# Kernel optimization log

Measured on AMD Instinct MI355X. Metric: run time of the kernel, lower is better.

The kernel has to match this reference:

```python
import jax, jax.numpy as jnp
import numpy as np

N = 50000   # input points
M = 50000   # output points
C = 32      # in_channels
H = 128     # hidden_dim
O = 64      # out_channels
E = 1_600_000  # total neighbor pairs (avg degree 32)


def setup_inputs() -> dict:
    key = jax.random.key(0)
    ks = jax.random.split(key, 6)
    in_features = jax.random.normal(ks[0], (N, C), jnp.float32)
    out_features = jax.random.normal(ks[1], (M, C), jnp.float32)
    neighbors_index = jax.random.randint(ks[2], (E,), 0, N, dtype=jnp.int32)
    rs = jnp.sort(jax.random.randint(ks[3], (M + 1,), 0, E, dtype=jnp.int32))
    neighbors_row_splits = rs.at[0].set(0).at[-1].set(E)
    W1 = jax.random.normal(ks[4], (2 * C, H), jnp.float32) / np.float32(np.sqrt(2 * C))
    b1 = jnp.zeros((H,), jnp.float32)
    W2 = jax.random.normal(ks[5], (H, O), jnp.float32) / np.float32(np.sqrt(H))
    b2 = jnp.zeros((O,), jnp.float32)
    return dict(in_features=in_features, out_features=out_features,
                W1=W1, b1=b1, W2=W2, b2=b2,
                neighbors_index=neighbors_index,
                neighbors_row_splits=neighbors_row_splits)


def reference(in_features, out_features, W1, b1, W2, b2,
              neighbors_index, neighbors_row_splits):
    rs = neighbors_row_splits
    counts = rs[1:] - rs[:-1]                      # [M] neighbors per output point
    # segment id of each edge: largest s with rs[s] <= e (handles empty segments)
    seg_ids = jnp.searchsorted(rs, jnp.arange(E, dtype=rs.dtype), side='right') - 1
    rep = in_features[neighbors_index]             # [E, C] gathered neighbor feats
    slf = out_features[seg_ids]                    # [E, C] == repeat_interleave(out, counts)
    agg = jnp.concatenate([rep, slf], axis=1)      # [E, 2C]
    h = jax.nn.gelu(agg @ W1 + b1, approximate=False)  # torch.nn.GELU is exact erf
    y = h @ W2 + b2                                # [E, O]
    summed = jax.ops.segment_sum(y, seg_ids, num_segments=M)  # [M, O]
    denom = jnp.maximum(counts, 1).astype(summed.dtype)[:, None]
    return summed / denom                          # segment_csr 'mean' (0 for empty)
```

## Files before the change

kernel.cpp:

```cpp
#include <hip/hip_runtime.h>
#include <hip/hip_bf16.h>

typedef __bf16 bf16_t;
typedef __attribute__((ext_vector_type(8))) __bf16 bf16x8;
typedef __attribute__((ext_vector_type(4))) float f32x4;
typedef __attribute__((ext_vector_type(4))) float float4_t;

#define MFMA16(a, b, c) __builtin_amdgcn_mfma_f32_16x16x32_bf16((a), (b), (c), 0, 0, 0)

__device__ __forceinline__ float gelu_fast(float x) {
    float z = x * fmaf(x * x, -0.1029453f, -2.3022081f);
    float e = __builtin_amdgcn_exp2f(z);
    return x * __builtin_amdgcn_rcpf(1.0f + e);
}

__device__ __forceinline__ int lbound(const int* __restrict__ a, int n, int v) {
    int lo = 0, hi = n;
    while (lo < hi) { int mid = (lo + hi) >> 1; if (a[mid] < v) lo = mid + 1; else hi = mid; }
    return lo;
}

__global__ __launch_bounds__(256, 2)
void nmlp_kernel(const float* __restrict__ in_f, const float* __restrict__ out_f,
                 const float* __restrict__ W1, const float* __restrict__ b1,
                 const float* __restrict__ W2, const float* __restrict__ b2,
                 const int* __restrict__ nbr, const int* __restrict__ rsp,
                 float* __restrict__ out, int M, int E, int epw)
{
    __shared__ alignas(16) unsigned char lds[32768];
    float* wstage = (float*)lds;
    const int tid = threadIdx.x, lane = tid & 63, wslot = tid >> 6;
    const int g = lane >> 4, c = lane & 15;

    {
        const float4_t* src = (const float4_t*)W1;
        float4_t* dst = (float4_t*)wstage;
        #pragma unroll
        for (int i = 0; i < 8; ++i) dst[tid + 256 * i] = src[tid + 256 * i];
    }
    __syncthreads();
    bf16x8 w1f[8][2];
    #pragma unroll
    for (int t = 0; t < 8; ++t)
        #pragma unroll
        for (int k = 0; k < 2; ++k)
            #pragma unroll
            for (int j = 0; j < 8; ++j)
                w1f[t][k][j] = (bf16_t)wstage[(32 * k + 8 * g + j) * 128 + 16 * t + c];
    __syncthreads();
    {
        const float4_t* src = (const float4_t*)W2;
        float4_t* dst = (float4_t*)wstage;
        #pragma unroll
        for (int i = 0; i < 8; ++i) dst[tid + 256 * i] = src[tid + 256 * i];
    }
    __syncthreads();
    bf16x8 w2f[4][4];
    #pragma unroll
    for (int u = 0; u < 4; ++u)
        #pragma unroll
        for (int k = 0; k < 4; ++k)
            #pragma unroll
            for (int j = 0; j < 8; ++j)
                w2f[u][k][j] = (bf16_t)wstage[(32 * k + 8 * g + j) * 64 + 16 * u + c];
    __syncthreads();

    float b1r[8], b2r[4];
    #pragma unroll
    for (int t = 0; t < 8; ++t) b1r[t] = b1[16 * t + c];
    #pragma unroll
    for (int u = 0; u < 4; ++u) b2r[u] = b2[16 * u + c];

    const unsigned hbase = (unsigned)wslot * 4352u;
    const unsigned hwb = hbase + (unsigned)(g * 1088 + 2 * c);
    const unsigned hrb = hbase + (unsigned)(c * 272 + 16 * g);

    const int wid = blockIdx.x * 4 + wslot;
    int sA = lbound(rsp, M + 1, wid * epw);
    int sB = lbound(rsp, M + 1, wid * epw + epw);
    if (sA > M) sA = M;
    if (sB > M) sB = M;
    if (sA >= sB) return;

    int s = sA;
    int e0c = rsp[s], e1c = rsp[s + 1];
    const int eS = e0c, eE = rsp[sB];

    f32x4 colacc[4];
    #pragma unroll
    for (int u = 0; u < 4; ++u) colacc[u] = (f32x4){0.f, 0.f, 0.f, 0.f};

    if (eS < eE) {
        int er = eS + c; if (er > eE - 1) er = eE - 1;
        int nb = nbr[er];
        int sg;
        { int lo2 = s, hi2 = sB - 1;
          while (lo2 < hi2) { int mid = (lo2 + hi2 + 1) >> 1; if (rsp[mid] <= er) lo2 = mid; else hi2 = mid - 1; }
          sg = lo2; }
        float4_t f0, f1, g0, g1;
        { const float4_t* rp = (const float4_t*)(in_f + (size_t)nb * 32 + 8 * g); f0 = rp[0]; f1 = rp[1]; }
        { const float4_t* sp = (const float4_t*)(out_f + (size_t)sg * 32 + 8 * g); g0 = sp[0]; g1 = sp[1]; }

        for (int et = eS; et < eE; et += 16) {
            const bool more = (et + 16 < eE);
            int nbN = 0, sgN = 0;
            if (more) {
                int erN = et + 16 + c; if (erN > eE - 1) erN = eE - 1;
                nbN = nbr[erN];
                int lo2 = s, hi2 = sB - 1;
                while (lo2 < hi2) { int mid = (lo2 + hi2 + 1) >> 1; if (rsp[mid] <= erN) lo2 = mid; else hi2 = mid - 1; }
                sgN = lo2;
            }
            bf16x8 a0, a1;
            #pragma unroll
            for (int j = 0; j < 4; ++j) {
                a0[j] = (bf16_t)f0[j]; a0[4 + j] = (bf16_t)f1[j];
                a1[j] = (bf16_t)g0[j]; a1[4 + j] = (bf16_t)g1[j];
            }
            #pragma unroll
            for (int t = 0; t < 8; ++t) {
                f32x4 h = {b1r[t], b1r[t], b1r[t], b1r[t]};
                h = MFMA16(a0, w1f[t][0], h);
                h = MFMA16(a1, w1f[t][1], h);
                #pragma unroll
                for (int j = 0; j < 4; ++j)
                    *(bf16_t*)(lds + hwb + j * 272 + t * 32) = (bf16_t)gelu_fast(h[j]);
            }
            if (more) {
                const float4_t* rp = (const float4_t*)(in_f + (size_t)nbN * 32 + 8 * g); f0 = rp[0]; f1 = rp[1];
                const float4_t* sp = (const float4_t*)(out_f + (size_t)sgN * 32 + 8 * g); g0 = sp[0]; g1 = sp[1];
            }
            const int tend = (et + 16 < eE) ? et + 16 : eE;
            const bool pure = (e0c <= et) && (e1c >= et + 16) && (et + 16 <= eE);
            if (pure) {
                #pragma unroll
                for (int k2 = 0; k2 < 4; ++k2) {
                    bf16x8 ah = *(const bf16x8*)(lds + hrb + k2 * 64);
                    #pragma unroll
                    for (int u = 0; u < 4; ++u) colacc[u] = MFMA16(ah, w2f[u][k2], colacc[u]);
                }
                while (e1c <= tend) {
                    const int d = e1c - e0c;
                    const float inv = (d > 0) ? __builtin_amdgcn_rcpf((float)d) : 0.0f;
                    float* orow = out + (size_t)s * 64;
                    #pragma unroll
                    for (int u = 0; u < 4; ++u) {
                        float v = colacc[u][0] + colacc[u][1] + colacc[u][2] + colacc[u][3];
                        v += __shfl_xor(v, 16); v += __shfl_xor(v, 32);
                        if (g == 0) orow[u * 16 + c] = (d > 0) ? v * inv + b2r[u] : 0.0f;
                        colacc[u] = (f32x4){0.f, 0.f, 0.f, 0.f};
                    }
                    ++s; e0c = e1c;
                    if (s >= sB) break;
                    e1c = rsp[s + 1];
                }
            } else {
                f32x4 y[4];
                #pragma unroll
                for (int u = 0; u < 4; ++u) y[u] = (f32x4){0.f, 0.f, 0.f, 0.f};
                #pragma unroll
                for (int k2 = 0; k2 < 4; ++k2) {
                    bf16x8 ah = *(const bf16x8*)(lds + hrb + k2 * 64);
                    #pragma unroll
                    for (int u = 0; u < 4; ++u) y[u] = MFMA16(ah, w2f[u][k2], y[u]);
                }
                while (true) {
                    int hi_p = ((e1c < tend) ? e1c : tend) - et;
                    int lo_p = e0c - et; if (lo_p < 0) lo_p = 0;
                    float m[4];
                    #pragma unroll
                    for (int j = 0; j < 4; ++j) {
                        int r = 4 * g + j;
                        m[j] = (r >= lo_p && r < hi_p) ? 1.0f : 0.0f;
                    }
                    #pragma unroll
                    for (int u = 0; u < 4; ++u)
                        #pragma unroll
                        for (int j = 0; j < 4; ++j)
                            colacc[u][j] = fmaf(y[u][j], m[j], colacc[u][j]);
                    if (e1c <= tend) {
                        const int d = e1c - e0c;
                        const float inv = (d > 0) ? __builtin_amdgcn_rcpf((float)d) : 0.0f;
                        float* orow = out + (size_t)s * 64;
                        #pragma unroll
                        for (int u = 0; u < 4; ++u) {
                            float v = colacc[u][0] + colacc[u][1] + colacc[u][2] + colacc[u][3];
                            v += __shfl_xor(v, 16); v += __shfl_xor(v, 32);
                            if (g == 0) orow[u * 16 + c] = (d > 0) ? v * inv + b2r[u] : 0.0f;
                            colacc[u] = (f32x4){0.f, 0.f, 0.f, 0.f};
                        }
                        ++s; e0c = e1c;
                        if (s >= sB) break;
                        e1c = rsp[s + 1];
                    } else break;
                }
            }
        }
    }
    while (s < sB) {
        float* orow = out + (size_t)s * 64;
        if (g == 0) {
            #pragma unroll
            for (int u = 0; u < 4; ++u) orow[u * 16 + c] = 0.0f;
        }
        ++s;
    }
}

extern "C" void kernel_launch(void* const* d_in, const int* in_sizes, int n_in,
                              void* d_out, int out_size, void* d_ws, size_t ws_size,
                              hipStream_t stream) {
    const float* in_f  = (const float*)d_in[0];
    const float* out_f = (const float*)d_in[1];
    const float* W1    = (const float*)d_in[2];
    const float* b1    = (const float*)d_in[3];
    const float* W2    = (const float*)d_in[4];
    const float* b2    = (const float*)d_in[5];
    const int*   nbr   = (const int*)d_in[6];
    const int*   rsp   = (const int*)d_in[7];
    float* out = (float*)d_out;
    const int M = in_sizes[7] - 1;
    const int E = in_sizes[6];

    const int nblocks = 1024;
    const int nwaves  = nblocks * 4;
    const int epw = (E + nwaves - 1) / nwaves;

    nmlp_kernel<<<dim3(nblocks), dim3(256), 0, stream>>>(in_f, out_f, W1, b1, W2, b2,
                                                         nbr, rsp, out, M, E, epw);
}
```

Before: 182.4 us.

## Keep weights in LDS in MFMA layout and process two 16-edge tiles per iteration

Weights are now stored as pre-swizzled bf16 fragments in LDS rather than held in registers. The MFMA operands are transposed so the hidden activations stay in registers and feed the second matmul directly, with no LDS round-trip. Each iteration processes two 16-edge tiles, and occupancy is raised to 3 blocks/SM with 768 blocks. The aim is lower register pressure, removal of the hidden-layer LDS staging and barrier traffic, and more memory latency hiding, at the cost of extra LDS weight reads per tile and a shuffle-based reduction at segment close.

```diff
diff --git a/kernel.cpp b/kernel.cpp
--- a/kernel.cpp
+++ b/kernel.cpp
@@ -20,188 +20,162 @@
     return lo;
 }
 
-__global__ __launch_bounds__(256, 2)
+__device__ __forceinline__ int seg_of(const int* __restrict__ rsp, int lo, int hi, int er) {
+    while (lo < hi) { int mid = (lo + hi + 1) >> 1; if (rsp[mid] <= er) lo = mid; else hi = mid - 1; }
+    return lo;
+}
+
+__global__ __launch_bounds__(256, 3)
 void nmlp_kernel(const float* __restrict__ in_f, const float* __restrict__ out_f,
                  const float* __restrict__ W1, const float* __restrict__ b1,
                  const float* __restrict__ W2, const float* __restrict__ b2,
                  const int* __restrict__ nbr, const int* __restrict__ rsp,
-                 float* __restrict__ out, int M, int E, int epw)
+                 float* __restrict__ out, int M, int E, int epw, int nwaves)
 {
-    __shared__ alignas(16) unsigned char lds[32768];
-    float* wstage = (float*)lds;
+    __shared__ alignas(16) unsigned char lds[33536];
     const int tid = threadIdx.x, lane = tid & 63, wslot = tid >> 6;
     const int g = lane >> 4, c = lane & 15;
 
-    {
-        const float4_t* src = (const float4_t*)W1;
-        float4_t* dst = (float4_t*)wstage;
-        #pragma unroll
-        for (int i = 0; i < 8; ++i) dst[tid + 256 * i] = src[tid + 256 * i];
-    }
+    for (int i = 0; i < 32; ++i) {
+        int idx = i * 256 + tid;
+        int k = idx >> 7, n = idx & 127;
+        int ks = k >> 5, gg = (k >> 3) & 3, j = k & 7, t = n >> 4, cc = n & 15;
+        ((bf16_t*)lds)[(((2 * t + ks) * 4 + gg) * 16 + cc) * 8 + j] = (bf16_t)W1[idx];
+    }
+    for (int i = 0; i < 32; ++i) {
+        int idx = i * 256 + tid;
+        int l = idx >> 6, o = idx & 63;
+        int t = l >> 4, gg = (l >> 2) & 3, j = l & 3;
+        int k2 = t >> 1, j2 = (t & 1) * 4 + j, u = o >> 4, cc = o & 15;
+        ((bf16_t*)lds)[8192 + (((u * 4 + k2) * 4 + gg) * 16 + cc) * 8 + j2] = (bf16_t)W2[idx];
+    }
+    if (tid < 128) *(float*)(lds + 32768 + tid * 4) = b1[tid];
+    if (tid < 64)  *(float*)(lds + 33280 + tid * 4) = b2[tid];
     __syncthreads();
-    bf16x8 w1f[8][2];
-    #pragma unroll
-    for (int t = 0; t < 8; ++t)
-        #pragma unroll
-        for (int k = 0; k < 2; ++k)
-            #pragma unroll
-            for (int j = 0; j < 8; ++j)
-                w1f[t][k][j] = (bf16_t)wstage[(32 * k + 8 * g + j) * 128 + 16 * t + c];
-    __syncthreads();
-    {
-        const float4_t* src = (const float4_t*)W2;
-        float4_t* dst = (float4_t*)wstage;
-        #pragma unroll
-        for (int i = 0; i < 8; ++i) dst[tid + 256 * i] = src[tid + 256 * i];
-    }
-    __syncthreads();
-    bf16x8 w2f[4][4];
-    #pragma unroll
-    for (int u = 0; u < 4; ++u)
-        #pragma unroll
-        for (int k = 0; k < 4; ++k)
-            #pragma unroll
-            for (int j = 0; j < 8; ++j)
-                w2f[u][k][j] = (bf16_t)wstage[(32 * k + 8 * g + j) * 64 + 16 * u + c];
-    __syncthreads();
-
-    float b1r[8], b2r[4];
-    #pragma unroll
-    for (int t = 0; t < 8; ++t) b1r[t] = b1[16 * t + c];
-    #pragma unroll
-    for (int u = 0; u < 4; ++u) b2r[u] = b2[16 * u + c];
-
-    const unsigned hbase = (unsigned)wslot * 4352u;
-    const unsigned hwb = hbase + (unsigned)(g * 1088 + 2 * c);
-    const unsigned hrb = hbase + (unsigned)(c * 272 + 16 * g);
+
+    const unsigned wbase = (unsigned)lane * 16u;
 
     const int wid = blockIdx.x * 4 + wslot;
     int sA = lbound(rsp, M + 1, wid * epw);
     int sB = lbound(rsp, M + 1, wid * epw + epw);
     if (sA > M) sA = M;
     if (sB > M) sB = M;
+    if (wid == nwaves - 1) sB = M;
     if (sA >= sB) return;
 
-    int s = sA;
-    int e0c = rsp[s], e1c = rsp[s + 1];
+    int s = sA, e0c = rsp[s], e1c = rsp[s + 1];
     const int eS = e0c, eE = rsp[sB];
 
     f32x4 colacc[4];
     #pragma unroll
     for (int u = 0; u < 4; ++u) colacc[u] = (f32x4){0.f, 0.f, 0.f, 0.f};
 
-    if (eS < eE) {
-        int er = eS + c; if (er > eE - 1) er = eE - 1;
-        int nb = nbr[er];
-        int sg;
-        { int lo2 = s, hi2 = sB - 1;
-          while (lo2 < hi2) { int mid = (lo2 + hi2 + 1) >> 1; if (rsp[mid] <= er) lo2 = mid; else hi2 = mid - 1; }
-          sg = lo2; }
-        float4_t f0, f1, g0, g1;
-        { const float4_t* rp = (const float4_t*)(in_f + (size_t)nb * 32 + 8 * g); f0 = rp[0]; f1 = rp[1]; }
-        { const float4_t* sp = (const float4_t*)(out_f + (size_t)sg * 32 + 8 * g); g0 = sp[0]; g1 = sp[1]; }
-
-        for (int et = eS; et < eE; et += 16) {
-            const bool more = (et + 16 < eE);
-            int nbN = 0, sgN = 0;
-            if (more) {
-                int erN = et + 16 + c; if (erN > eE - 1) erN = eE - 1;
-                nbN = nbr[erN];
-                int lo2 = s, hi2 = sB - 1;
-                while (lo2 < hi2) { int mid = (lo2 + hi2 + 1) >> 1; if (rsp[mid] <= erN) lo2 = mid; else hi2 = mid - 1; }
-                sgN = lo2;
-            }
-            bf16x8 a0, a1;
-            #pragma unroll
-            for (int j = 0; j < 4; ++j) {
-                a0[j] = (bf16_t)f0[j]; a0[4 + j] = (bf16_t)f1[j];
-                a1[j] = (bf16_t)g0[j]; a1[4 + j] = (bf16_t)g1[j];
-            }
-            #pragma unroll
-            for (int t = 0; t < 8; ++t) {
-                f32x4 h = {b1r[t], b1r[t], b1r[t], b1r[t]};
-                h = MFMA16(a0, w1f[t][0], h);
-                h = MFMA16(a1, w1f[t][1], h);
+    auto accum_close = [&](int bt, const f32x4* y) {
+        const int tend = (bt + 16 < eE) ? bt + 16 : eE;
+        const int er = bt + c;
+        while (true) {
+            int hi_p = (e1c < tend) ? e1c : tend;
+            int lo_p = (e0c > bt) ? e0c : bt;
+            float m = (er >= lo_p && er < hi_p) ? 1.0f : 0.0f;
+            #pragma unroll
+            for (int u = 0; u < 4; ++u)
                 #pragma unroll
                 for (int j = 0; j < 4; ++j)
-                    *(bf16_t*)(lds + hwb + j * 272 + t * 32) = (bf16_t)gelu_fast(h[j]);
-            }
-            if (more) {
-                const float4_t* rp = (const float4_t*)(in_f + (size_t)nbN * 32 + 8 * g); f0 = rp[0]; f1 = rp[1];
-                const float4_t* sp = (const float4_t*)(out_f + (size_t)sgN * 32 + 8 * g); g0 = sp[0]; g1 = sp[1];
-            }
-            const int tend = (et + 16 < eE) ? et + 16 : eE;
-            const bool pure = (e0c <= et) && (e1c >= et + 16) && (et + 16 <= eE);
-            if (pure) {
-                #pragma unroll
-                for (int k2 = 0; k2 < 4; ++k2) {
-                    bf16x8 ah = *(const bf16x8*)(lds + hrb + k2 * 64);
-                    #pragma unroll
-                    for (int u = 0; u < 4; ++u) colacc[u] = MFMA16(ah, w2f[u][k2], colacc[u]);
-                }
-                while (e1c <= tend) {
-                    const int d = e1c - e0c;
-                    const float inv = (d > 0) ? __builtin_amdgcn_rcpf((float)d) : 0.0f;
-                    float* orow = out + (size_t)s * 64;
-                    #pragma unroll
-                    for (int u = 0; u < 4; ++u) {
-                        float v = colacc[u][0] + colacc[u][1] + colacc[u][2] + colacc[u][3];
-                        v += __shfl_xor(v, 16); v += __shfl_xor(v, 32);
-                        if (g == 0) orow[u * 16 + c] = (d > 0) ? v * inv + b2r[u] : 0.0f;
-                        colacc[u] = (f32x4){0.f, 0.f, 0.f, 0.f};
-                    }
-                    ++s; e0c = e1c;
-                    if (s >= sB) break;
-                    e1c = rsp[s + 1];
-                }
-            } else {
-                f32x4 y[4];
-                #pragma unroll
-                for (int u = 0; u < 4; ++u) y[u] = (f32x4){0.f, 0.f, 0.f, 0.f};
-                #pragma unroll
-                for (int k2 = 0; k2 < 4; ++k2) {
-                    bf16x8 ah = *(const bf16x8*)(lds + hrb + k2 * 64);
-                    #pragma unroll
-                    for (int u = 0; u < 4; ++u) y[u] = MFMA16(ah, w2f[u][k2], y[u]);
-                }
-                while (true) {
-                    int hi_p = ((e1c < tend) ? e1c : tend) - et;
-                    int lo_p = e0c - et; if (lo_p < 0) lo_p = 0;
-                    float m[4];
+                    colacc[u][j] = fmaf(y[u][j], m, colacc[u][j]);
+            if (e1c <= tend) {
+                const int d = e1c - e0c;
+                const float inv = (d > 0) ? __builtin_amdgcn_rcpf((float)d) : 0.0f;
+                float* orow = out + (size_t)s * 64;
+                #pragma unroll
+                for (int u = 0; u < 4; ++u) {
+                    const f32x4 b2v = *(const f32x4*)(lds + 33280 + u * 64 + g * 16);
                     #pragma unroll
                     for (int j = 0; j < 4; ++j) {
-                        int r = 4 * g + j;
-                        m[j] = (r >= lo_p && r < hi_p) ? 1.0f : 0.0f;
+                        float v = colacc[u][j];
+                        v += __shfl_xor(v, 1); v += __shfl_xor(v, 2);
+                        v += __shfl_xor(v, 4); v += __shfl_xor(v, 8);
+                        if (c == 0) orow[u * 16 + g * 4 + j] = (d > 0) ? fmaf(v, inv, b2v[j]) : 0.0f;
                     }
-                    #pragma unroll
-                    for (int u = 0; u < 4; ++u)
-                        #pragma unroll
-                        for (int j = 0; j < 4; ++j)
-                            colacc[u][j] = fmaf(y[u][j], m[j], colacc[u][j]);
-                    if (e1c <= tend) {
-                        const int d = e1c - e0c;
-                        const float inv = (d > 0) ? __builtin_amdgcn_rcpf((float)d) : 0.0f;
-                        float* orow = out + (size_t)s * 64;
-                        #pragma unroll
-                        for (int u = 0; u < 4; ++u) {
-                            float v = colacc[u][0] + colacc[u][1] + colacc[u][2] + colacc[u][3];
-                            v += __shfl_xor(v, 16); v += __shfl_xor(v, 32);
-                            if (g == 0) orow[u * 16 + c] = (d > 0) ? v * inv + b2r[u] : 0.0f;
-                            colacc[u] = (f32x4){0.f, 0.f, 0.f, 0.f};
-                        }
-                        ++s; e0c = e1c;
-                        if (s >= sB) break;
-                        e1c = rsp[s + 1];
-                    } else break;
+                    colacc[u] = (f32x4){0.f, 0.f, 0.f, 0.f};
                 }
-            }
+                ++s; e0c = e1c;
+                if (s >= sB) break;
+                e1c = rsp[s + 1];
+            } else break;
+        }
+    };
+
+    if (eS < eE) {
+        int erA = eS + c;      if (erA > eE - 1) erA = eE - 1;
+        int erB = eS + 16 + c; if (erB > eE - 1) erB = eE - 1;
+        int nbA = nbr[erA], nbB = nbr[erB];
+        int sgA = seg_of(rsp, s, sB - 1, erA), sgB = seg_of(rsp, s, sB - 1, erB);
+        float4_t fA0, fA1, gA0, gA1, fB0, fB1, gB0, gB1;
+        { const float4_t* p = (const float4_t*)(in_f  + (size_t)nbA * 32 + 8 * g); fA0 = p[0]; fA1 = p[1]; }
+        { const float4_t* p = (const float4_t*)(out_f + (size_t)sgA * 32 + 8 * g); gA0 = p[0]; gA1 = p[1]; }
+        { const float4_t* p = (const float4_t*)(in_f  + (size_t)nbB * 32 + 8 * g); fB0 = p[0]; fB1 = p[1]; }
+        { const float4_t* p = (const float4_t*)(out_f + (size_t)sgB * 32 + 8 * g); gB0 = p[0]; gB1 = p[1]; }
+
+        for (int et = eS; et < eE; et += 32) {
+            bf16x8 aA0, aA1, aB0, aB1;
+            #pragma unroll
+            for (int j = 0; j < 4; ++j) {
+                aA0[j] = (bf16_t)fA0[j]; aA0[4 + j] = (bf16_t)fA1[j];
+                aA1[j] = (bf16_t)gA0[j]; aA1[4 + j] = (bf16_t)gA1[j];
+                aB0[j] = (bf16_t)fB0[j]; aB0[4 + j] = (bf16_t)fB1[j];
+                aB1[j] = (bf16_t)gB0[j]; aB1[4 + j] = (bf16_t)gB1[j];
+            }
+            const bool more = (et + 32 < eE);
+            int nbA2 = 0, sgA2 = 0, nbB2 = 0, sgB2 = 0;
+            if (more) {
+                int eA2 = et + 32 + c; if (eA2 > eE - 1) eA2 = eE - 1;
+                int eB2 = et + 48 + c; if (eB2 > eE - 1) eB2 = eE - 1;
+                nbA2 = nbr[eA2]; nbB2 = nbr[eB2];
+                sgA2 = seg_of(rsp, s, sB - 1, eA2); sgB2 = seg_of(rsp, s, sB - 1, eB2);
+            }
+            bf16x8 phA[4], phB[4];
+            #pragma unroll
+            for (int t = 0; t < 8; ++t) {
+                const f32x4 b1v  = *(const f32x4*)(lds + 32768 + t * 64 + g * 16);
+                const bf16x8 w10 = *(const bf16x8*)(lds + wbase + (2 * t) * 1024);
+                const bf16x8 w11 = *(const bf16x8*)(lds + wbase + (2 * t + 1) * 1024);
+                f32x4 hA = b1v, hB = b1v;
+                hA = MFMA16(w10, aA0, hA); hA = MFMA16(w11, aA1, hA);
+                hB = MFMA16(w10, aB0, hB); hB = MFMA16(w11, aB1, hB);
+                #pragma unroll
+                for (int j = 0; j < 4; ++j) {
+                    phA[t >> 1][(t & 1) * 4 + j] = (bf16_t)gelu_fast(hA[j]);
+                    phB[t >> 1][(t & 1) * 4 + j] = (bf16_t)gelu_fast(hB[j]);
+                }
+            }
+            if (more) {
+                { const float4_t* p = (const float4_t*)(in_f  + (size_t)nbA2 * 32 + 8 * g); fA0 = p[0]; fA1 = p[1]; }
+                { const float4_t* p = (const float4_t*)(out_f + (size_t)sgA2 * 32 + 8 * g); gA0 = p[0]; gA1 = p[1]; }
+                { const float4_t* p = (const float4_t*)(in_f  + (size_t)nbB2 * 32 + 8 * g); fB0 = p[0]; fB1 = p[1]; }
+                { const float4_t* p = (const float4_t*)(out_f + (size_t)sgB2 * 32 + 8 * g); gB0 = p[0]; gB1 = p[1]; }
+            }
+            f32x4 yA[4], yB[4];
+            #pragma unroll
+            for (int u = 0; u < 4; ++u) { yA[u] = (f32x4){0.f,0.f,0.f,0.f}; yB[u] = (f32x4){0.f,0.f,0.f,0.f}; }
+            #pragma unroll
+            for (int u = 0; u < 4; ++u)
+                #pragma unroll
+                for (int k2 = 0; k2 < 4; ++k2) {
+                    const bf16x8 w2 = *(const bf16x8*)(lds + 16384 + wbase + (u * 4 + k2) * 1024);
+                    yA[u] = MFMA16(w2, phA[k2], yA[u]);
+                    yB[u] = MFMA16(w2, phB[k2], yB[u]);
+                }
+            accum_close(et, yA);
+            if (et + 16 < eE) accum_close(et + 16, yB);
         }
     }
     while (s < sB) {
         float* orow = out + (size_t)s * 64;
-        if (g == 0) {
-            #pragma unroll
-            for (int u = 0; u < 4; ++u) orow[u * 16 + c] = 0.0f;
+        if (c == 0) {
+            #pragma unroll
+            for (int u = 0; u < 4; ++u)
+                #pragma unroll
+                for (int j = 0; j < 4; ++j) orow[u * 16 + g * 4 + j] = 0.0f;
         }
         ++s;
     }
@@ -222,10 +196,10 @@
     const int M = in_sizes[7] - 1;
     const int E = in_sizes[6];
 
-    const int nblocks = 1024;
+    const int nblocks = 768;
     const int nwaves  = nblocks * 4;
     const int epw = (E + nwaves - 1) / nwaves;
 
     nmlp_kernel<<<dim3(nblocks), dim3(256), 0, stream>>>(in_f, out_f, W1, b1, W2, b2,
-                                                         nbr, rsp, out, M, E, epw);
-}
+                                                         nbr, rsp, out, M, E, epw, nwaves);
+}
```

Result: slower. 570.6 us (+212.9%).
